# Kernel tuning notes

Hardware: AMD Instinct MI355X
Metric: run time of the kernel (lower is better)

## Reference

```python
import jax, jax.numpy as jnp
import numpy as np

E = 512; V = 50257; BLOCK = 1024; H = 8; L = 4
HS = E // H
EPS = 1e-5


def _ln(x, g, b):
    mu = x.mean(-1, keepdims=True)
    var = ((x - mu) ** 2).mean(-1, keepdims=True)
    return (x - mu) * jax.lax.rsqrt(var + EPS) * g + b


def setup_inputs() -> dict:
    key = jax.random.key(0)
    ks = jax.random.split(key, 24)
    B, T = 4, 1024
    std = 0.02
    inp = {
        'idx': jax.random.randint(ks[0], (B, T), 0, V, dtype=jnp.int64) if jax.config.jax_enable_x64 else jax.random.randint(ks[0], (B, T), 0, V, dtype=jnp.int32),
        'targets': jax.random.randint(ks[1], (B, T), 0, V, dtype=jnp.int32),
        'attention_mask': jnp.ones((B, T), dtype=jnp.int32),
        'tok_emb': jax.random.normal(ks[2], (V, E), jnp.float32) * std,
        'pos_emb': jax.random.normal(ks[3], (BLOCK, E), jnp.float32) * std,
        'wq': jax.random.normal(ks[4], (L, H, E, HS), jnp.float32) * std,
        'wk': jax.random.normal(ks[5], (L, H, E, HS), jnp.float32) * std,
        'wv': jax.random.normal(ks[6], (L, H, E, HS), jnp.float32) * std,
        'bq': jnp.zeros((L, H, HS), jnp.float32),
        'bk': jnp.zeros((L, H, HS), jnp.float32),
        'bv': jnp.zeros((L, H, HS), jnp.float32),
        'wo': jax.random.normal(ks[7], (L, E, E), jnp.float32) * std,
        'bo': jnp.zeros((L, E), jnp.float32),
        'ln1_g': jnp.ones((L, E), jnp.float32),
        'ln1_b': jnp.zeros((L, E), jnp.float32),
        'ln2_g': jnp.ones((L, E), jnp.float32),
        'ln2_b': jnp.zeros((L, E), jnp.float32),
        'w1': jax.random.normal(ks[8], (L, E, 4 * E), jnp.float32) * std,
        'b1': jnp.zeros((L, 4 * E), jnp.float32),
        'w2': jax.random.normal(ks[9], (L, 4 * E, E), jnp.float32) * std,
        'b2': jnp.zeros((L, E), jnp.float32),
        'lnf_g': jnp.ones((E,), jnp.float32),
        'lnf_b': jnp.zeros((E,), jnp.float32),
        'wf': jax.random.normal(ks[10], (E, V), jnp.float32) * std,
        'bf': jnp.zeros((V,), jnp.float32),
    }
    return inp


def reference(idx, targets, attention_mask, tok_emb, pos_emb, wq, wk, wv, bq, bk, bv,
              wo, bo, ln1_g, ln1_b, ln2_g, ln2_b, w1, b1, w2, b2, lnf_g, lnf_b, wf, bf):
    B, T = idx.shape
    x = tok_emb[idx] + pos_emb[:T]  # [B,T,E]
    causal = jnp.tril(jnp.ones((T, T), dtype=bool))[None, None]           # [1,1,T,T]
    keymask = (attention_mask != 0)[:, None, None, :]                      # [B,1,1,T]
    mask = causal & keymask                                                # [B,1,T,T]
    scale = HS ** -0.5
    neg_inf = jnp.float32(-jnp.inf)
    for l in range(L):
        h = _ln(x, ln1_g[l], ln1_b[l])
        q = jnp.einsum('bte,heo->bhto', h, wq[l]) + bq[l][None, :, None, :]
        k = jnp.einsum('bte,heo->bhto', h, wk[l]) + bk[l][None, :, None, :]
        v = jnp.einsum('bte,heo->bhto', h, wv[l]) + bv[l][None, :, None, :]
        wei = jnp.einsum('bhqd,bhkd->bhqk', q, k) * scale
        wei = jnp.where(mask, wei, neg_inf)
        att = jax.nn.softmax(wei, axis=-1)
        o = jnp.einsum('bhqk,bhkd->bhqd', att, v)
        o = o.transpose(0, 2, 1, 3).reshape(B, T, H * HS)  # concat heads
        x = x + o @ wo[l] + bo[l]
        h2 = _ln(x, ln2_g[l], ln2_b[l])
        x = x + jax.nn.relu(h2 @ w1[l] + b1[l]) @ w2[l] + b2[l]
    x = _ln(x, lnf_g, lnf_b)
    logits = (x @ wf + bf).reshape(B * T, V)
    logp = jax.nn.log_softmax(logits, axis=-1)
    loss = -jnp.take_along_axis(logp, targets.reshape(-1, 1), axis=-1).mean()
    return logits, loss
```

## Files before the change

kernel.cpp:

```cpp
#include <hip/hip_runtime.h>
#include <math.h>

#define E 512
#define V 50257
#define T 1024
#define B 4
#define H 8
#define HS 64
#define L 4
#define FF 2048
#define NTOK 4096

#define NPAD 50304
#define KSPL 1024

typedef _Float16 f16;
typedef _Float16 f16x8 __attribute__((ext_vector_type(8)));
typedef float    f32x4 __attribute__((ext_vector_type(4)));

__device__ inline float wave_max(float v){ for(int o=32;o;o>>=1) v=fmaxf(v,__shfl_xor(v,o)); return v; }
__device__ inline float wave_sum(float v){ for(int o=32;o;o>>=1) v+=__shfl_xor(v,o); return v; }

__device__ inline void lse_merge(float& m, float& s, float m2, float s2){
  float mn = fmaxf(m, m2);
  if (mn == -INFINITY){ m = mn; s = 0.f; return; }
  s = s*__expf(m - mn) + s2*__expf(m2 - mn);
  m = mn;
}

__global__ __launch_bounds__(256) void embed_ln_split_kernel(const int* __restrict__ idx,
    const float* __restrict__ tok, const float* __restrict__ pos,
    const float* __restrict__ g, const float* __restrict__ bb,
    float* __restrict__ X, f16* __restrict__ A2){
  int row = blockIdx.x; int tid = threadIdx.x;
  int t = row & (T-1);
  const float* te = tok + (size_t)idx[row]*E;
  const float* pe = pos + (size_t)t*E;
  float v0 = te[tid] + pe[tid];
  float v1 = te[tid+256] + pe[tid+256];
  float* xr = X + (size_t)row*E;
  xr[tid] = v0; xr[tid+256] = v1;
  int wave = tid>>6, lane = tid&63;
  __shared__ float r1[4], r2[4];
  float s = wave_sum(v0+v1);
  if (!lane) r1[wave]=s;
  __syncthreads();
  float mean = (r1[0]+r1[1]+r1[2]+r1[3]) * (1.f/E);
  float d0=v0-mean, d1=v1-mean;
  float vs = wave_sum(d0*d0+d1*d1);
  if (!lane) r2[wave]=vs;
  __syncthreads();
  float var = (r2[0]+r2[1]+r2[2]+r2[3]) * (1.f/E);
  float rs = rsqrtf(var + 1e-5f);
  float y0 = d0*rs*g[tid]     + bb[tid];
  float y1 = d1*rs*g[tid+256] + bb[tid+256];
  size_t base = (size_t)row*KSPL;
  f16 h0=(f16)y0, h1=(f16)y1;
  A2[base + tid]         = h0;
  A2[base + E + tid]     = (f16)(y0 - (float)h0);
  A2[base + tid+256]     = h1;
  A2[base + E + tid+256] = (f16)(y1 - (float)h1);
}

__global__ __launch_bounds__(256) void red4_ln_split_kernel(const float* __restrict__ P,
    const float* __restrict__ bias, const float* __restrict__ g, const float* __restrict__ bb,
    float* __restrict__ X, f16* __restrict__ A2){
  int row = blockIdx.x; int tid = threadIdx.x;
  const size_t STRIDE = (size_t)NTOK*E;
  size_t i0 = (size_t)row*E + tid, i1 = i0 + 256;
  float v0 = X[i0] + P[i0] + P[i0+STRIDE] + P[i0+2*STRIDE] + P[i0+3*STRIDE] + bias[tid];
  float v1 = X[i1] + P[i1] + P[i1+STRIDE] + P[i1+2*STRIDE] + P[i1+3*STRIDE] + bias[tid+256];
  X[i0] = v0; X[i1] = v1;
  int wave = tid>>6, lane = tid&63;
  __shared__ float r1[4], r2[4];
  float s = wave_sum(v0+v1);
  if (!lane) r1[wave]=s;
  __syncthreads();
  float mean = (r1[0]+r1[1]+r1[2]+r1[3]) * (1.f/E);
  float d0=v0-mean, d1=v1-mean;
  float vs = wave_sum(d0*d0+d1*d1);
  if (!lane) r2[wave]=vs;
  __syncthreads();
  float var = (r2[0]+r2[1]+r2[2]+r2[3]) * (1.f/E);
  float rs = rsqrtf(var + 1e-5f);
  float y0 = d0*rs*g[tid]     + bb[tid];
  float y1 = d1*rs*g[tid+256] + bb[tid+256];
  size_t base = (size_t)row*KSPL;
  f16 h0=(f16)y0, h1=(f16)y1;
  A2[base + tid]         = h0;
  A2[base + E + tid]     = (f16)(y0 - (float)h0);
  A2[base + tid+256]     = h1;
  A2[base + E + tid+256] = (f16)(y1 - (float)h1);
}

__global__ __launch_bounds__(256) void ln_kernel(const float* __restrict__ X,
    const float* __restrict__ g, const float* __restrict__ bb, float* __restrict__ O){
  int row = blockIdx.x; int tid = threadIdx.x;
  const float* x = X + (size_t)row*E;
  float v0 = x[tid], v1 = x[tid+256];
  int wave = tid>>6, lane = tid&63;
  __shared__ float r1[4], r2[4];
  float s = wave_sum(v0+v1);
  if (!lane) r1[wave]=s;
  __syncthreads();
  float mean = (r1[0]+r1[1]+r1[2]+r1[3]) * (1.f/E);
  float d0=v0-mean, d1=v1-mean;
  float vs = wave_sum(d0*d0+d1*d1);
  if (!lane) r2[wave]=vs;
  __syncthreads();
  float var = (r2[0]+r2[1]+r2[2]+r2[3]) * (1.f/E);
  float rs = rsqrtf(var + 1e-5f);
  float* o = O + (size_t)row*E;
  o[tid]     = d0*rs*g[tid]     + bb[tid];
  o[tid+256] = d1*rs*g[tid+256] + bb[tid+256];
}

template<bool RELU, bool RESID>
__global__ __launch_bounds__(256) void sgemm(const float* __restrict__ A, const float* __restrict__ Bm,
    const float* __restrict__ bias, const float* __restrict__ Rs, float* __restrict__ C,
    int M, int N, int K, int Hn,
    long long sA, long long sB, long long sBias, long long sC){
  int z = blockIdx.z;
  A    += (long long)(z / Hn) * sA;
  Bm   += (long long)(z % Hn) * sB;
  bias += (long long)(z % Hn) * sBias;
  C    += (long long)z * sC;
  __shared__ float As[16][68];
  __shared__ float Bs[16][64];
  int tid = threadIdx.x;
  int tx = tid & 15, ty = tid >> 4;
  int m0 = blockIdx.y * 64, n0 = blockIdx.x * 64;
  int ar = tid >> 2, ac = (tid & 3) << 2;
  int br = tid >> 4, bc = (tid & 15) << 2;
  float acc[4][4] = {};
  const float* Ap = A + (size_t)(m0+ar)*K + ac;
  const float* Bp = Bm + (size_t)br*N + n0 + bc;
  int bn = n0 + bc;
  for (int k0=0; k0<K; k0+=16){
    float4 av = *(const float4*)Ap;
    As[ac+0][ar]=av.x; As[ac+1][ar]=av.y; As[ac+2][ar]=av.z; As[ac+3][ar]=av.w;
    float4 bv;
    if (bn+3 < N) bv = *(const float4*)Bp;
    else {
      bv.x = (bn+0<N)?Bp[0]:0.f; bv.y=(bn+1<N)?Bp[1]:0.f;
      bv.z = (bn+2<N)?Bp[2]:0.f; bv.w=(bn+3<N)?Bp[3]:0.f;
    }
    *(float4*)&Bs[br][bc] = bv;
    __syncthreads();
    #pragma unroll
    for (int kk=0; kk<16; ++kk){
      float4 a4 = *(const float4*)&As[kk][ty<<2];
      float4 b4 = *(const float4*)&Bs[kk][tx<<2];
      acc[0][0] = fmaf(a4.x,b4.x,acc[0][0]); acc[0][1] = fmaf(a4.x,b4.y,acc[0][1]);
      acc[0][2] = fmaf(a4.x,b4.z,acc[0][2]); acc[0][3] = fmaf(a4.x,b4.w,acc[0][3]);
      acc[1][0] = fmaf(a4.y,b4.x,acc[1][0]); acc[1][1] = fmaf(a4.y,b4.y,acc[1][1]);
      acc[1][2] = fmaf(a4.y,b4.z,acc[1][2]); acc[1][3] = fmaf(a4.y,b4.w,acc[1][3]);
      acc[2][0] = fmaf(a4.z,b4.x,acc[2][0]); acc[2][1] = fmaf(a4.z,b4.y,acc[2][1]);
      acc[2][2] = fmaf(a4.z,b4.z,acc[2][2]); acc[2][3] = fmaf(a4.z,b4.w,acc[2][3]);
      acc[3][0] = fmaf(a4.w,b4.x,acc[3][0]); acc[3][1] = fmaf(a4.w,b4.y,acc[3][1]);
      acc[3][2] = fmaf(a4.w,b4.z,acc[3][2]); acc[3][3] = fmaf(a4.w,b4.w,acc[3][3]);
    }
    __syncthreads();
    Ap += 16; Bp += (size_t)16*N;
  }
  #pragma unroll
  for (int i=0;i<4;++i){
    int row = m0 + (ty<<2) + i;
    float* crow = C + (size_t)row*N;
    #pragma unroll
    for (int j=0;j<4;++j){
      int col = n0 + (tx<<2) + j;
      if (col < N){
        float vv = acc[i][j] + bias[col];
        if (RESID) vv += Rs[(size_t)row*N + col];
        if (RELU)  vv = fmaxf(vv, 0.f);
        crow[col] = vv;
      }
    }
  }
}


#define GLOBAL_AS __attribute__((address_space(1)))
#define LDS_AS    __attribute__((address_space(3)))

__device__ inline void gll16(const void* g, void* l){
  __builtin_amdgcn_global_load_lds((const GLOBAL_AS void*)g, (LDS_AS void*)l, 16, 0, 0);
}

__global__ __launch_bounds__(256) void split_w_f16(const float* __restrict__ W,
    f16* __restrict__ B1, int N, int K){
  __shared__ float S[64][65];
  int n0 = blockIdx.x * 64;
  int k0 = blockIdx.y * 64;
  int t = threadIdx.x;
  #pragma unroll
  for (int p=0;p<16;++p){
    int e = p*256 + t;
    int kl = e >> 6, nl = e & 63;
    S[kl][nl] = W[(size_t)(k0+kl)*N + n0+nl];
  }
  __syncthreads();
  #pragma unroll
  for (int p=0;p<16;++p){
    int e = p*256 + t;
    int nl = e >> 6, kl = e & 63;
    B1[(size_t)(n0+nl)*(size_t)K + (k0+kl)] = (f16)S[kl][nl];
  }
}

__global__ __launch_bounds__(256) void split_wqkv_f16(const float* __restrict__ wq,
    const float* __restrict__ wk, const float* __restrict__ wv, f16* __restrict__ B1,
    const float* __restrict__ bq, const float* __restrict__ bk, const float* __restrict__ bv,
    float* __restrict__ bqkv){
  if (blockIdx.x == 0 && blockIdx.y == 0){
    for (int i=threadIdx.x; i<1536; i+=256)
      bqkv[i] = (i < 512) ? bq[i] : (i < 1024 ? bk[i-512] : bv[i-1024]);
  }
  __shared__ float S[64][65];
  int n0 = blockIdx.x * 64;
  int e0 = blockIdx.y * 64;
  const float* W; int nloc;
  if (n0 < 512){ W = wq; nloc = n0; }
  else if (n0 < 1024){ W = wk; nloc = n0 - 512; }
  else { W = wv; nloc = n0 - 1024; }
  int h = nloc >> 6;
  int t = threadIdx.x;
  #pragma unroll
  for (int p=0;p<16;++p){
    int idx2 = p*256 + t;
    int e = idx2 >> 6, o = idx2 & 63;
    S[e][o] = W[((size_t)(h*E + e0 + e))*HS + o];
  }
  __syncthreads();
  #pragma unroll
  for (int p=0;p<16;++p){
    int idx2 = p*256 + t;
    int r = idx2 >> 6, c = idx2 & 63;
    B1[(size_t)(n0 + r)*512 + (e0 + c)] = (f16)S[c][r];
  }
}

__global__ __launch_bounds__(256) void split_bT_f16(const float* __restrict__ Wf, f16* __restrict__ B1){
  __shared__ float S[64][65];
  int n0 = blockIdx.x * 64;
  int k0 = blockIdx.y * 64;
  int t = threadIdx.x;
  #pragma unroll
  for (int p=0;p<16;++p){
    int e = p*256 + t;
    int kl = e >> 6, nl = e & 63;
    int n = n0 + nl;
    S[kl][nl] = (n < V) ? Wf[(size_t)(k0+kl)*V + n] : 0.f;
  }
  __syncthreads();
  #pragma unroll
  for (int p=0;p<16;++p){
    int e = p*256 + t;
    int nl = e >> 6, kl = e & 63;
    B1[(size_t)(n0+nl)*512 + (k0+kl)] = (f16)S[kl][nl];
  }
}

template<bool RELU, bool OUTSPLIT, bool PARTIAL4, int K, int NLOG>
__global__ __launch_bounds__(256) void mfma_gemm_f16(
    const f16* __restrict__ A2, const f16* __restrict__ B1,
    const float* __restrict__ bias, float* __restrict__ C, f16* __restrict__ C2){
  __shared__ f16 As[128*64];
  __shared__ f16 Bs[128*64];
  int tid = threadIdx.x;
  int lane = tid & 63, wv = tid >> 6;
  int wm = wv >> 1, wn = wv & 1;
  int m0 = blockIdx.x * 128;
  int n0 = blockIdx.y * 128;

  f32x4 acc[4][4];
  #pragma unroll
  for (int i=0;i<4;++i)
    #pragma unroll
    for (int j=0;j<4;++j){ f32x4 z = {0.f,0.f,0.f,0.f}; acc[i][j] = z; }

  constexpr size_t LDA = (size_t)(4*K);
  constexpr size_t LDB = (size_t)(2*K);
  const char* Abase = (const char*)A2 + (size_t)m0*LDA;
  const char* Bbase = (const char*)B1 + (size_t)n0*LDB;
  int halfm = wm*64, halfn = wn*64;

  constexpr int NPS = PARTIAL4 ? 1 : 2;
  constexpr int KRANGE = PARTIAL4 ? (K/2) : K;
  int kbase = PARTIAL4 ? ((int)blockIdx.z & 1)*(K/2) : 0;
  #pragma unroll
  for (int pi=0; pi<NPS; ++pi){
    int term = PARTIAL4 ? ((int)blockIdx.z >> 1) : pi;
    size_t abyte = ((size_t)term*K + (size_t)kbase)*2;
    size_t bbyte = (size_t)kbase*2;
    for (int kk=0; kk<KRANGE; kk+=64){
      const char* Ak = Abase + abyte + (size_t)kk*2;
      const char* Bk = Bbase + bbyte + (size_t)kk*2;
      #pragma unroll
      for (int p=0;p<4;++p){
        int slot = p*256 + tid;
        int row  = slot >> 3;
        int sch  = (slot & 7) ^ (row & 7);
        gll16(Ak + (size_t)row*LDA + (sch<<4), (char*)As + (p<<12) + (wv<<10));
      }
      #pragma unroll
      for (int p=0;p<4;++p){
        int slot = p*256 + tid;
        int row  = slot >> 3;
        int sch  = (slot & 7) ^ (row & 7);
        gll16(Bk + (size_t)row*LDB + (sch<<4), (char*)Bs + (p<<12) + (wv<<10));
      }
      __syncthreads();
      #pragma unroll
      for (int kp=0; kp<2; ++kp){
        f16x8 af[4], bfr[4];
        int chq = kp*4 + (lane >> 4);
        #pragma unroll
        for (int mf=0; mf<4; ++mf){
          int r = halfm + mf*16 + (lane & 15);
          int sch = chq ^ (r & 7);
          af[mf] = *(const f16x8*)((const char*)As + r*128 + (sch<<4));
        }
        #pragma unroll
        for (int nf=0; nf<4; ++nf){
          int r = halfn + nf*16 + (lane & 15);
          int sch = chq ^ (r & 7);
          bfr[nf] = *(const f16x8*)((const char*)Bs + r*128 + (sch<<4));
        }
        #pragma unroll
        for (int mf=0; mf<4; ++mf)
          #pragma unroll
          for (int nf=0; nf<4; ++nf)
            acc[mf][nf] = __builtin_amdgcn_mfma_f32_16x16x32_f16(af[mf], bfr[nf], acc[mf][nf], 0, 0, 0);
      }
      __syncthreads();
    }
  }
  float* Cp = C;
  if (PARTIAL4) Cp += (size_t)blockIdx.z * ((size_t)NTOK*NLOG);
  #pragma unroll
  for (int mf=0; mf<4; ++mf){
    int row = m0 + halfm + mf*16 + ((lane>>4)<<2);
    #pragma unroll
    for (int nf=0; nf<4; ++nf){
      int col = n0 + halfn + nf*16 + (lane & 15);
      if (col < NLOG){
        #pragma unroll
        for (int r=0;r<4;++r){
          float vv = acc[mf][nf][r];
          if (PARTIAL4){
            Cp[(size_t)(row+r)*NLOG + col] = vv;
          } else if (OUTSPLIT){
            vv += bias[col];
            if (RELU) vv = fmaxf(vv, 0.f);
            f16 h = (f16)vv;
            C2[(size_t)(row+r)*(2*(size_t)NLOG) + col]        = h;
            C2[(size_t)(row+r)*(2*(size_t)NLOG) + NLOG + col] = (f16)(vv - (float)h);
          } else {
            vv += bias[col];
            if (RELU) vv = fmaxf(vv, 0.f);
            Cp[(size_t)(row+r)*NLOG + col] = vv;
          }
        }
      }
    }
  }
}

__global__ __launch_bounds__(256) void attn_fused_kernel(const float* __restrict__ QKV,
    const int* __restrict__ amask, f16* __restrict__ A2out){
  int blk = blockIdx.x;
  int qc = blk & 255;
  int bh = blk >> 8;
  int b = bh >> 3, h = bh & 7;
  int wave = threadIdx.x >> 6, lane = threadIdx.x & 63;
  int qi = (qc<<2) + wave;
  __shared__ float Ks[64][68];
  __shared__ float Vs[64][68];
  __shared__ float Ps[4][64];
  __shared__ int   Ms[64];
  const float* qrow = QKV + (size_t)(b*T + qi)*1536 + (h<<6);
  float4 qreg[16];
  #pragma unroll
  for (int d4=0; d4<16; ++d4) qreg[d4] = *(const float4*)(qrow + (d4<<2));
  const float* kb = QKV + (size_t)(b*T)*1536 + 512 + (h<<6);
  float acc=0.f, m=-INFINITY, l=0.f;
  int nchunk = (((qc<<2)+3)>>6) + 1;
  for (int c=0;c<nchunk;++c){
    __syncthreads();
    #pragma unroll
    for (int i=0;i<4;++i){
      int fi = threadIdx.x + i*256;
      int r = fi >> 4, f4 = fi & 15;
      const float* krow = kb + (size_t)(c*64 + r)*1536 + (f4<<2);
      float4 kv = *(const float4*)krow;
      float4 vv = *(const float4*)(krow + 512);
      int cc = f4 << 2;
      *(float4*)&Ks[r][cc] = kv;
      *(float4*)&Vs[r][cc] = vv;
    }
    if (threadIdx.x < 64) Ms[threadIdx.x] = amask[b*T + (c<<6) + threadIdx.x];
    __syncthreads();
    int kidx = (c<<6) + lane;
    bool valid = (kidx <= qi) && (Ms[lane] != 0);
    float dot = 0.f;
    #pragma unroll
    for (int d4=0; d4<16; ++d4){
      float4 k4 = *(const float4*)&Ks[lane][d4<<2];
      dot = fmaf(qreg[d4].x, k4.x, dot);
      dot = fmaf(qreg[d4].y, k4.y, dot);
      dot = fmaf(qreg[d4].z, k4.z, dot);
      dot = fmaf(qreg[d4].w, k4.w, dot);
    }
    float s = valid ? dot * 0.125f : -INFINITY;
    float cm = wave_max(s);
    float mnew = fmaxf(m, cm);
    float corr = (mnew > -INFINITY) ? __expf(m - mnew) : 0.f;
    float p = valid ? __expf(s - mnew) : 0.f;
    float ps = wave_sum(p);
    l = l*corr + ps;
    acc *= corr;
    Ps[wave][lane] = p;
    #pragma unroll
    for (int k4=0; k4<16; ++k4){
      float4 p4 = *(const float4*)&Ps[wave][k4<<2];
      int k0 = k4 << 2;
      acc = fmaf(p4.x, Vs[k0+0][lane], acc);
      acc = fmaf(p4.y, Vs[k0+1][lane], acc);
      acc = fmaf(p4.z, Vs[k0+2][lane], acc);
      acc = fmaf(p4.w, Vs[k0+3][lane], acc);
    }
    m = mnew;
  }
  float o = acc / l;
  f16 hh = (f16)o;
  size_t base = (size_t)(b*T + qi)*KSPL + (h<<6) + lane;
  A2out[base]     = hh;
  A2out[base + E] = (f16)(o - (float)hh);
}

__global__ __launch_bounds__(256) void attn_kernel(const float* __restrict__ Q,
    const float* __restrict__ Kg, const float* __restrict__ Vg,
    const int* __restrict__ amask, float* __restrict__ O){
  int blk = blockIdx.x;
  int qc = blk & 255;
  int bh = blk >> 8;
  int b = bh >> 3, h = bh & 7;
  int wave = threadIdx.x >> 6, lane = threadIdx.x & 63;
  int qi = (qc<<2) + wave;
  __shared__ float Ks[64][65];
  __shared__ float Vs[64][65];
  __shared__ float Qs[4][64];
  __shared__ int   Ms[64];
  const float* qp = Q + ((size_t)bh*T + qi)*HS;
  Qs[wave][lane] = qp[lane];
  const float* kb = Kg + (size_t)bh*T*HS;
  const float* vb = Vg + (size_t)bh*T*HS;
  float acc=0.f, m=-INFINITY, l=0.f;
  int nchunk = (((qc<<2)+3)>>6) + 1;
  for (int c=0;c<nchunk;++c){
    __syncthreads();
    #pragma unroll
    for (int i=0;i<4;++i){
      int fi = threadIdx.x + i*256;
      int r = fi >> 4, cc = (fi & 15) << 2;
      float4 kv = *(const float4*)(kb + (size_t)c*4096 + ((size_t)fi<<2));
      Ks[r][cc]=kv.x; Ks[r][cc+1]=kv.y; Ks[r][cc+2]=kv.z; Ks[r][cc+3]=kv.w;
      float4 vv = *(const float4*)(vb + (size_t)c*4096 + ((size_t)fi<<2));
      Vs[r][cc]=vv.x; Vs[r][cc+1]=vv.y; Vs[r][cc+2]=vv.z; Vs[r][cc+3]=vv.w;
    }
    if (threadIdx.x < 64) Ms[threadIdx.x] = amask[b*T + (c<<6) + threadIdx.x];
    __syncthreads();
    int kidx = (c<<6) + lane;
    bool valid = (kidx <= qi) && (Ms[lane] != 0);
    float dot = 0.f;
    #pragma unroll
    for (int d=0; d<64; ++d) dot = fmaf(Qs[wave][d], Ks[lane][d], dot);
    float s = valid ? dot * 0.125f : -INFINITY;
    float cm = wave_max(s);
    float mnew = fmaxf(m, cm);
    float corr = (mnew > -INFINITY) ? __expf(m - mnew) : 0.f;
    float p = valid ? __expf(s - mnew) : 0.f;
    float ps = wave_sum(p);
    l = l*corr + ps;
    acc *= corr;
    #pragma unroll
    for (int k2=0;k2<64;++k2){
      float pk = __shfl(p, k2);
      acc = fmaf(pk, Vs[k2][lane], acc);
    }
    m = mnew;
  }
  O[((size_t)b*T + qi)*E + (h<<6) + lane] = acc / l;
}

__global__ __launch_bounds__(256) void loss_row(const float* __restrict__ logits,
    const int* __restrict__ tgt, float* __restrict__ part){
  int row = blockIdx.x; int tid = threadIdx.x;
  const float* lr = logits + (size_t)row*V;
  float m = -INFINITY, s = 0.f;
  for (int i=tid; i<V; i+=256){
    float x = lr[i];
    if (x > m){ s = s*__expf(m - x) + 1.f; m = x; }
    else s += __expf(x - m);
  }
  for (int o=32;o;o>>=1){
    float m2 = __shfl_xor(m,o), s2 = __shfl_xor(s,o);
    lse_merge(m, s, m2, s2);
  }
  int wave=tid>>6, lane=tid&63;
  __shared__ float sm[4], ss[4];
  if (!lane){ sm[wave]=m; ss[wave]=s; }
  __syncthreads();
  if (tid==0){
    float M = sm[0], S = ss[0];
    lse_merge(M, S, sm[1], ss[1]);
    lse_merge(M, S, sm[2], ss[2]);
    lse_merge(M, S, sm[3], ss[3]);
    part[row] = M + __logf(S) - lr[tgt[row]];
  }
}

__global__ __launch_bounds__(256) void loss_final(const float* __restrict__ part, float* __restrict__ out){
  int tid = threadIdx.x;
  float s=0.f;
  for (int i=tid;i<NTOK;i+=256) s += part[i];
  s = wave_sum(s);
  __shared__ float sr[4];
  int wave=tid>>6, lane=tid&63;
  if (!lane) sr[wave]=s;
  __syncthreads();
  if (tid==0) out[0] = (sr[0]+sr[1]+sr[2]+sr[3]) * (1.f/NTOK);
}

__global__ __launch_bounds__(256) void embed_kernel(const int* __restrict__ idx,
    const float* __restrict__ tok, const float* __restrict__ pos, float* __restrict__ X){
  int i = blockIdx.x*256 + threadIdx.x;
  int e = i & (E-1);
  int bt = i >> 9;
  int t = bt & (T-1);
  X[i] = tok[(size_t)idx[bt]*E + e] + pos[t*E + e];
}

extern "C" void kernel_launch(void* const* d_in, const int* in_sizes, int n_in,
                              void* d_out, int out_size, void* d_ws, size_t ws_size,
                              hipStream_t stream) {
  const int*   idx    = (const int*)  d_in[0];
  const int*   tgt    = (const int*)  d_in[1];
  const int*   amask  = (const int*)  d_in[2];
  const float* tok    = (const float*)d_in[3];
  const float* pos    = (const float*)d_in[4];
  const float* wq     = (const float*)d_in[5];
  const float* wk     = (const float*)d_in[6];
  const float* wv     = (const float*)d_in[7];
  const float* bq     = (const float*)d_in[8];
  const float* bk     = (const float*)d_in[9];
  const float* bv     = (const float*)d_in[10];
  const float* wo     = (const float*)d_in[11];
  const float* bo     = (const float*)d_in[12];
  const float* ln1g   = (const float*)d_in[13];
  const float* ln1b   = (const float*)d_in[14];
  const float* ln2g   = (const float*)d_in[15];
  const float* ln2b   = (const float*)d_in[16];
  const float* w1     = (const float*)d_in[17];
  const float* b1     = (const float*)d_in[18];
  const float* w2     = (const float*)d_in[19];
  const float* b2     = (const float*)d_in[20];
  const float* lnfg   = (const float*)d_in[21];
  const float* lnfb   = (const float*)d_in[22];
  const float* wf     = (const float*)d_in[23];
  const float* bf     = (const float*)d_in[24];

  char* wsb = (char*)d_ws;
  float* out = (float*)d_out;

  const size_t SZ = (size_t)NTOK*E;
  const size_t OLD_BYTES = (6*SZ + (size_t)NTOK*FF + NTOK)*sizeof(float);
  bool use_mfma = (ws_size >= OLD_BYTES);

  float* X = (float*)wsb;

  if (use_mfma){
    float* QKV    = (float*)(wsb + 16777216);
    float* P4     = (float*)(wsb + 16777216);
    f16*   A2a    = (f16*)  (wsb + 50331648);
    f16*   U2     = (f16*)  (wsb + 58720256);
    f16*   B2qkv  = (f16*)  (wsb + 92274688);
    f16*   B2wo   = (f16*)  (wsb + 95420416);
    f16*   B2w1   = (f16*)  (wsb + 96468992);
    f16*   B2w2   = (f16*)  (wsb + 100663296);
    float* bqkv   = (float*)(wsb + 104857600);
    const size_t B2SP_BYTES = (size_t)NPAD*512*2;
    f16*   B2sp   = (f16*)wsb;
    f16*   A2sp   = (f16*)(wsb + B2SP_BYTES);
    float* PART2  = (float*)(wsb + B2SP_BYTES + (size_t)NTOK*KSPL*2);

    embed_ln_split_kernel<<<NTOK, 256, 0, stream>>>(idx, tok, pos, ln1g, ln1b, X, A2a);

    for (int l=0; l<L; ++l){
      split_wqkv_f16<<<dim3(24,8), 256, 0, stream>>>(
          wq + (size_t)l*H*E*HS, wk + (size_t)l*H*E*HS, wv + (size_t)l*H*E*HS, B2qkv,
          bq + (size_t)l*H*HS, bk + (size_t)l*H*HS, bv + (size_t)l*H*HS, bqkv);
      mfma_gemm_f16<false,false,false,512,1536><<<dim3(32,12,1), 256, 0, stream>>>(
          A2a, B2qkv, bqkv, QKV, nullptr);
      attn_fused_kernel<<<B*H*(T/4), 256, 0, stream>>>(QKV, amask, A2a);
      split_w_f16<<<dim3(8,8), 256, 0, stream>>>(wo + (size_t)l*E*E, B2wo, 512, 512);
      mfma_gemm_f16<false,false,true,512,512><<<dim3(32,4,4), 256, 0, stream>>>(
          A2a, B2wo, nullptr, P4, nullptr);
      red4_ln_split_kernel<<<NTOK, 256, 0, stream>>>(
          P4, bo + (size_t)l*E, ln2g + (size_t)l*E, ln2b + (size_t)l*E, X, A2a);
      split_w_f16<<<dim3(32,8), 256, 0, stream>>>(w1 + (size_t)l*E*FF, B2w1, 2048, 512);
      mfma_gemm_f16<true,true,false,512,2048><<<dim3(32,16,1), 256, 0, stream>>>(
          A2a, B2w1, b1 + (size_t)l*FF, nullptr, U2);
      split_w_f16<<<dim3(8,32), 256, 0, stream>>>(w2 + (size_t)l*FF*E, B2w2, 512, 2048);
      mfma_gemm_f16<false,false,true,2048,512><<<dim3(32,4,4), 256, 0, stream>>>(
          U2, B2w2, nullptr, P4, nullptr);
      if (l < L-1){
        red4_ln_split_kernel<<<NTOK, 256, 0, stream>>>(
            P4, b2 + (size_t)l*E, ln1g + (size_t)(l+1)*E, ln1b + (size_t)(l+1)*E, X, A2a);
      } else {
        red4_ln_split_kernel<<<NTOK, 256, 0, stream>>>(
            P4, b2 + (size_t)l*E, lnfg, lnfb, X, A2sp);
      }
    }

    split_bT_f16<<<dim3(NPAD/64, E/64, 1), 256, 0, stream>>>(wf, B2sp);
    mfma_gemm_f16<false,false,false,512,V><<<dim3(NTOK/128, NPAD/128, 1), 256, 0, stream>>>(
        A2sp, B2sp, bf, out, nullptr);
    loss_row<<<NTOK, 256, 0, stream>>>(out, tgt, PART2);
    loss_final<<<1, 256, 0, stream>>>(PART2, out + (size_t)NTOK*V);
  } else {
    float* ws  = (float*)d_ws;
    float* Hb  = ws + 1*SZ;
    float* Qb  = ws + 2*SZ;
    float* Kb  = ws + 3*SZ;
    float* Vb  = ws + 4*SZ;
    float* ATT = ws + 5*SZ;
    float* U   = ws + 6*SZ;
    float* PART= ws + 6*SZ + (size_t)NTOK*FF;

    embed_kernel<<<NTOK*E/256, 256, 0, stream>>>(idx, tok, pos, X);
    for (int l=0; l<L; ++l){
      ln_kernel<<<NTOK, 256, 0, stream>>>(X, ln1g + (size_t)l*E, ln1b + (size_t)l*E, Hb);
      sgemm<false,false><<<dim3(1,T/64,B*H), 256, 0, stream>>>(
          Hb, wq + (size_t)l*H*E*HS, bq + (size_t)l*H*HS, nullptr, Qb,
          T, HS, E, H, (long long)T*E, (long long)E*HS, (long long)HS, (long long)T*HS);
      sgemm<false,false><<<dim3(1,T/64,B*H), 256, 0, stream>>>(
          Hb, wk + (size_t)l*H*E*HS, bk + (size_t)l*H*HS, nullptr, Kb,
          T, HS, E, H, (long long)T*E, (long long)E*HS, (long long)HS, (long long)T*HS);
      sgemm<false,false><<<dim3(1,T/64,B*H), 256, 0, stream>>>(
          Hb, wv + (size_t)l*H*E*HS, bv + (size_t)l*H*HS, nullptr, Vb,
          T, HS, E, H, (long long)T*E, (long long)E*HS, (long long)HS, (long long)T*HS);
      attn_kernel<<<B*H*(T/4), 256, 0, stream>>>(Qb, Kb, Vb, amask, ATT);
      sgemm<false,true><<<dim3(E/64, NTOK/64, 1), 256, 0, stream>>>(
          ATT, wo + (size_t)l*E*E, bo + (size_t)l*E, X, X,
          NTOK, E, E, 1, 0,0,0,0);
      ln_kernel<<<NTOK, 256, 0, stream>>>(X, ln2g + (size_t)l*E, ln2b + (size_t)l*E, Hb);
      sgemm<true,false><<<dim3(FF/64, NTOK/64, 1), 256, 0, stream>>>(
          Hb, w1 + (size_t)l*E*FF, b1 + (size_t)l*FF, nullptr, U,
          NTOK, FF, E, 1, 0,0,0,0);
      sgemm<false,true><<<dim3(E/64, NTOK/64, 1), 256, 0, stream>>>(
          U, w2 + (size_t)l*FF*E, b2 + (size_t)l*E, X, X,
          NTOK, E, FF, 1, 0,0,0,0);
    }
    ln_kernel<<<NTOK, 256, 0, stream>>>(X, lnfg, lnfb, Hb);
    sgemm<false,false><<<dim3((V+63)/64, NTOK/64, 1), 256, 0, stream>>>(
        Hb, wf, bf, nullptr, out, NTOK, V, E, 1, 0,0,0,0);
    loss_row<<<NTOK, 256, 0, stream>>>(out, tgt, PART);
    loss_final<<<1, 256, 0, stream>>>(PART, out + (size_t)NTOK*V);
  }
}
```

Measured before the change: 2.462 ms.

## Load A hi/lo split halves together to reuse B tile across both terms

The GEMM kernel previously streamed the A high and low f16 halves in two separate passes, each reloading the same B tile. It now loads both A halves plus one B tile per K step and issues MFMAs for both terms against the shared B fragments. This halves B global traffic and the number of barriers. In exchange it adds 16KB of shared memory, which may reduce occupancy. The split-K partial path now partitions K into quarters instead of term×half.

```diff
diff --git a/kernel.cpp b/kernel.cpp
--- a/kernel.cpp
+++ b/kernel.cpp
@@ -262,11 +262,12 @@
   }
 }
 
-template<bool RELU, bool OUTSPLIT, bool PARTIAL4, int K, int NLOG>
+template<bool RELU, bool OUTSPLIT, bool PARTIAL, int K, int NLOG>
 __global__ __launch_bounds__(256) void mfma_gemm_f16(
     const f16* __restrict__ A2, const f16* __restrict__ B1,
     const float* __restrict__ bias, float* __restrict__ C, f16* __restrict__ C2){
-  __shared__ f16 As[128*64];
+  __shared__ f16 Ah[128*64];
+  __shared__ f16 Al[128*64];
   __shared__ f16 Bs[128*64];
   int tid = threadIdx.x;
   int lane = tid & 63, wv = tid >> 6;
@@ -286,59 +287,71 @@
   const char* Bbase = (const char*)B1 + (size_t)n0*LDB;
   int halfm = wm*64, halfn = wn*64;
 
-  constexpr int NPS = PARTIAL4 ? 1 : 2;
-  constexpr int KRANGE = PARTIAL4 ? (K/2) : K;
-  int kbase = PARTIAL4 ? ((int)blockIdx.z & 1)*(K/2) : 0;
-  #pragma unroll
-  for (int pi=0; pi<NPS; ++pi){
-    int term = PARTIAL4 ? ((int)blockIdx.z >> 1) : pi;
-    size_t abyte = ((size_t)term*K + (size_t)kbase)*2;
-    size_t bbyte = (size_t)kbase*2;
-    for (int kk=0; kk<KRANGE; kk+=64){
-      const char* Ak = Abase + abyte + (size_t)kk*2;
-      const char* Bk = Bbase + bbyte + (size_t)kk*2;
+  constexpr int KRANGE = PARTIAL ? (K/4) : K;
+  int kbase = PARTIAL ? (int)blockIdx.z * (K/4) : 0;
+  for (int kk=0; kk<KRANGE; kk+=64){
+    const char* Akh = Abase + (size_t)(kbase + kk)*2;
+    const char* Akl = Abase + (size_t)(K + kbase + kk)*2;
+    const char* Bk  = Bbase + (size_t)(kbase + kk)*2;
+    #pragma unroll
+    for (int p=0;p<4;++p){
+      int slot = p*256 + tid;
+      int row  = slot >> 3;
+      int sch  = (slot & 7) ^ (row & 7);
+      gll16(Akh + (size_t)row*LDA + (sch<<4), (char*)Ah + (p<<12) + (wv<<10));
+    }
+    #pragma unroll
+    for (int p=0;p<4;++p){
+      int slot = p*256 + tid;
+      int row  = slot >> 3;
+      int sch  = (slot & 7) ^ (row & 7);
+      gll16(Akl + (size_t)row*LDA + (sch<<4), (char*)Al + (p<<12) + (wv<<10));
+    }
+    #pragma unroll
+    for (int p=0;p<4;++p){
+      int slot = p*256 + tid;
+      int row  = slot >> 3;
+      int sch  = (slot & 7) ^ (row & 7);
+      gll16(Bk + (size_t)row*LDB + (sch<<4), (char*)Bs + (p<<12) + (wv<<10));
+    }
+    __syncthreads();
+    #pragma unroll
+    for (int kp=0; kp<2; ++kp){
+      f16x8 af[4], bfr[4];
+      int chq = kp*4 + (lane >> 4);
       #pragma unroll
-      for (int p=0;p<4;++p){
-        int slot = p*256 + tid;
-        int row  = slot >> 3;
-        int sch  = (slot & 7) ^ (row & 7);
-        gll16(Ak + (size_t)row*LDA + (sch<<4), (char*)As + (p<<12) + (wv<<10));
+      for (int nf=0; nf<4; ++nf){
+        int r = halfn + nf*16 + (lane & 15);
+        int sch = chq ^ (r & 7);
+        bfr[nf] = *(const f16x8*)((const char*)Bs + r*128 + (sch<<4));
       }
       #pragma unroll
-      for (int p=0;p<4;++p){
-        int slot = p*256 + tid;
-        int row  = slot >> 3;
-        int sch  = (slot & 7) ^ (row & 7);
-        gll16(Bk + (size_t)row*LDB + (sch<<4), (char*)Bs + (p<<12) + (wv<<10));
+      for (int mf=0; mf<4; ++mf){
+        int r = halfm + mf*16 + (lane & 15);
+        int sch = chq ^ (r & 7);
+        af[mf] = *(const f16x8*)((const char*)Ah + r*128 + (sch<<4));
       }
-      __syncthreads();
       #pragma unroll
-      for (int kp=0; kp<2; ++kp){
-        f16x8 af[4], bfr[4];
-        int chq = kp*4 + (lane >> 4);
+      for (int mf=0; mf<4; ++mf)
         #pragma unroll
-        for (int mf=0; mf<4; ++mf){
-          int r = halfm + mf*16 + (lane & 15);
-          int sch = chq ^ (r & 7);
-          af[mf] = *(const f16x8*)((const char*)As + r*128 + (sch<<4));
-        }
+        for (int nf=0; nf<4; ++nf)
+          acc[mf][nf] = __builtin_amdgcn_mfma_f32_16x16x32_f16(af[mf], bfr[nf], acc[mf][nf], 0, 0, 0);
+      #pragma unroll
+      for (int mf=0; mf<4; ++mf){
+        int r = halfm + mf*16 + (lane & 15);
+        int sch = chq ^ (r & 7);
+        af[mf] = *(const f16x8*)((const char*)Al + r*128 + (sch<<4));
+      }
+      #pragma unroll
+      for (int mf=0; mf<4; ++mf)
         #pragma unroll
-        for (int nf=0; nf<4; ++nf){
-          int r = halfn + nf*16 + (lane & 15);
-          int sch = chq ^ (r & 7);
-          bfr[nf] = *(const f16x8*)((const char*)Bs + r*128 + (sch<<4));
-        }
-        #pragma unroll
-        for (int mf=0; mf<4; ++mf)
-          #pragma unroll
-          for (int nf=0; nf<4; ++nf)
-            acc[mf][nf] = __builtin_amdgcn_mfma_f32_16x16x32_f16(af[mf], bfr[nf], acc[mf][nf], 0, 0, 0);
-      }
-      __syncthreads();
-    }
+        for (int nf=0; nf<4; ++nf)
+          acc[mf][nf] = __builtin_amdgcn_mfma_f32_16x16x32_f16(af[mf], bfr[nf], acc[mf][nf], 0, 0, 0);
+    }
+    __syncthreads();
   }
   float* Cp = C;
-  if (PARTIAL4) Cp += (size_t)blockIdx.z * ((size_t)NTOK*NLOG);
+  if (PARTIAL) Cp += (size_t)blockIdx.z * ((size_t)NTOK*NLOG);
   #pragma unroll
   for (int mf=0; mf<4; ++mf){
     int row = m0 + halfm + mf*16 + ((lane>>4)<<2);
@@ -349,7 +362,7 @@
         #pragma unroll
         for (int r=0;r<4;++r){
           float vv = acc[mf][nf][r];
-          if (PARTIAL4){
+          if (PARTIAL){
             Cp[(size_t)(row+r)*NLOG + col] = vv;
           } else if (OUTSPLIT){
             vv += bias[col];
```

Measured after the change: 2.480 ms. Within noise of the previous version (+0.7%).
